# Kernel tuning notes

Hardware: AMD Instinct MI355X
Metric: run time of the kernel (lower is better)

The kernel has to match this reference:

```python
import jax, jax.numpy as jnp
import numpy as np

B, N, QD = 2, 4096, 512
HEADS, DIM_HEAD = 8, 64
INNER = HEADS * DIM_HEAD  # 512
SCALE = DIM_HEAD ** -0.5


def setup_inputs() -> dict:
    key = jax.random.key(0)
    ks = jax.random.split(key, 6)
    s = 0.02
    return {
        "x": jax.random.normal(ks[0], (B, N, QD), dtype=jnp.float32),
        "Wq": jax.random.normal(ks[1], (QD, INNER), dtype=jnp.float32) * s,
        "Wk": jax.random.normal(ks[2], (QD, INNER), dtype=jnp.float32) * s,
        "Wv": jax.random.normal(ks[3], (QD, INNER), dtype=jnp.float32) * s,
        "Wo": jax.random.normal(ks[4], (INNER, QD), dtype=jnp.float32) * s,
        "bo": jnp.zeros((QD,), dtype=jnp.float32),
    }


def reference(x, Wq, Wk, Wv, Wo, bo):
    # self-attention: context = x; mask = None; attention_sf = False
    q = x @ Wq  # [B, N, INNER]
    k = x @ Wk
    v = x @ Wv
    # split heads: [B, H, N, D]
    def split(t):
        return t.reshape(B, N, HEADS, DIM_HEAD).transpose(0, 2, 1, 3)
    q, k, v = split(q), split(k), split(v)
    # fp32 QK^T (ATTN_PRECISION='fp32' path)
    sim = jnp.einsum('bhid,bhjd->bhij', q.astype(jnp.float32), k.astype(jnp.float32)) * SCALE
    attn = jax.nn.softmax(sim, axis=-1)
    out = jnp.einsum('bhij,bhjd->bhid', attn, v)  # [B, H, N, D]
    out = out.transpose(0, 2, 1, 3).reshape(B, N, INNER)
    return out @ Wo + bo  # Dropout(p=0) is identity
```

## Files before the change

kernel.cpp:

```cpp
#include <hip/hip_runtime.h>
#include <hip/hip_bf16.h>


typedef __attribute__((ext_vector_type(8))) short short8;
typedef __attribute__((ext_vector_type(4))) float floatx4;
typedef __attribute__((ext_vector_type(16))) float floatx16;

#define MFMA16(a, b, c) __builtin_amdgcn_mfma_f32_16x16x32_bf16((a), (b), (c), 0, 0, 0)
#define MFMA32(a, b, c) __builtin_amdgcn_mfma_f32_32x32x16_bf16((a), (b), (c), 0, 0, 0)

#if __has_builtin(__builtin_amdgcn_exp2f)
#define EXP2(x) __builtin_amdgcn_exp2f(x)
#else
#define EXP2(x) exp2f(x)
#endif

#define QSCALE 0.18033688011112042f

static __device__ __forceinline__ unsigned short f2b(float f) {
  unsigned int u = __float_as_uint(f);
  u += 0x7FFFu + ((u >> 16) & 1u);
  return (unsigned short)(u >> 16);
}

static __device__ __forceinline__ unsigned int pkb(float a, float b) {
  float2 t{a, b};
  __hip_bfloat162 h = __float22bfloat162_rn(t);
  union { __hip_bfloat162 h2; unsigned int u; } cv;
  cv.h2 = h;
  return cv.u;
}

static __device__ __forceinline__ void dma16(const unsigned short* g,
                                             unsigned short* l) {
  __builtin_amdgcn_global_load_lds(
      (const __attribute__((address_space(1))) unsigned int*)g,
      (__attribute__((address_space(3))) unsigned int*)l, 16, 0, 0);
}

__global__ __launch_bounds__(256) void prep_kernel(
    const float* __restrict__ Wq, const float* __restrict__ Wk,
    const float* __restrict__ Wv, const float* __restrict__ Wo,
    const float* __restrict__ x, unsigned short* __restrict__ wtq,
    unsigned short* __restrict__ wtk, unsigned short* __restrict__ wtv,
    unsigned short* __restrict__ wto, unsigned short* __restrict__ xb) {
  const int z = blockIdx.z;
  const int tid = threadIdx.x;
  if (z >= 4) {
    const int bid = (z - 4) * 256 + blockIdx.y * 16 + blockIdx.x;
    const int idx = (bid * 256 + tid) * 8;
    const float4 a = *(const float4*)(x + idx);
    const float4 b = *(const float4*)(x + idx + 4);
    unsigned int u[4] = {pkb(a.x, a.y), pkb(a.z, a.w), pkb(b.x, b.y),
                         pkb(b.z, b.w)};
    *(short8*)(xb + idx) = *(short8*)u;
    return;
  }
  const float* __restrict__ W = (z == 0) ? Wq : (z == 1) ? Wk : (z == 2) ? Wv : Wo;
  unsigned short* __restrict__ T = (z == 0) ? wtq : (z == 1) ? wtk : (z == 2) ? wtv : wto;
  const int k0 = blockIdx.x * 32, c0 = blockIdx.y * 32;
  __shared__ float Ts[32][33];
  const int r = tid >> 3, cc = (tid & 7) * 4;
  const float4 v = *(const float4*)(W + (k0 + r) * 512 + c0 + cc);
  Ts[r][cc] = v.x; Ts[r][cc + 1] = v.y; Ts[r][cc + 2] = v.z; Ts[r][cc + 3] = v.w;
  __syncthreads();
  const unsigned long long uu =
      (unsigned long long)pkb(Ts[cc][r], Ts[cc + 1][r]) |
      ((unsigned long long)pkb(Ts[cc + 2][r], Ts[cc + 3][r]) << 32);
  *(unsigned long long*)(T + (c0 + r) * 512 + k0 + cc) = uu;
}

__global__ __launch_bounds__(256) void qkv_fused_kernel(
    const unsigned short* __restrict__ xb, const unsigned short* __restrict__ wtq,
    const unsigned short* __restrict__ wtk,
    const unsigned short* __restrict__ wtv, unsigned short* __restrict__ qo,
    unsigned short* __restrict__ ko, unsigned short* __restrict__ vo) {
  const int m0 = blockIdx.x * 128;
  const int c0 = blockIdx.y * 32;
  __shared__ __align__(16) unsigned short As[2][128 * 64];
  __shared__ __align__(16) unsigned short Bs[2][3][32 * 64];
  const int tid = threadIdx.x;
  const int lane = tid & 63, w = tid >> 6;
  const int i = lane & 15, q = lane >> 4;
  const int sl = i & 7;
  const int dr = lane >> 3, dc = lane & 7;
  const int sch = (dc ^ dr) * 8;
  const unsigned short* ag = xb + (m0 + w * 32 + dr) * 512 + sch;
  const unsigned short* bg[3];
  bg[0] = wtq + (c0 + w * 8 + dr) * 512 + sch;
  bg[1] = wtk + (c0 + w * 8 + dr) * 512 + sch;
  bg[2] = wtv + (c0 + w * 8 + dr) * 512 + sch;

  floatx4 acc[3][2][2] = {};

#pragma unroll
  for (int p = 0; p < 4; ++p) dma16(ag + p * 8 * 512, &As[0][(w * 32 + p * 8) * 64]);
#pragma unroll
  for (int z = 0; z < 3; ++z) dma16(bg[z], &Bs[0][z][(w * 8) * 64]);
  __syncthreads();

  int buf = 0;
  for (int ks = 0; ks < 8; ++ks) {
    if (ks < 7) {
      const int k1 = (ks + 1) * 64;
#pragma unroll
      for (int p = 0; p < 4; ++p)
        dma16(ag + p * 8 * 512 + k1, &As[buf ^ 1][(w * 32 + p * 8) * 64]);
#pragma unroll
      for (int z = 0; z < 3; ++z)
        dma16(bg[z] + k1, &Bs[buf ^ 1][z][(w * 8) * 64]);
    }
#pragma unroll
    for (int kc = 0; kc < 2; ++kc) {
      short8 af[2];
#pragma unroll
      for (int t = 0; t < 2; ++t)
        af[t] = *(const short8*)&As[buf][(w * 32 + t * 16 + i) * 64 +
                                        (((kc * 4 + q) ^ sl) * 8)];
#pragma unroll
      for (int z = 0; z < 3; ++z)
#pragma unroll
        for (int g = 0; g < 2; ++g) {
          const short8 bf = *(const short8*)&Bs[buf][z][(g * 16 + i) * 64 +
                                                        (((kc * 4 + q) ^ sl) * 8)];
#pragma unroll
          for (int t = 0; t < 2; ++t)
            acc[z][t][g] = MFMA16(af[t], bf, acc[z][t][g]);
        }
    }
    __syncthreads();
    buf ^= 1;
  }
#pragma unroll
  for (int z = 0; z < 3; ++z)
#pragma unroll
    for (int t = 0; t < 2; ++t)
#pragma unroll
      for (int g = 0; g < 2; ++g) {
        const int col = c0 + g * 16 + i;
        const int h = col >> 6, d = col & 63;
        const int row0 = m0 + w * 32 + t * 16 + q * 4;
        const int b = row0 >> 12;
        const int n0 = row0 & 4095;
        if (z == 2) {
          unsigned int* dst =
              (unsigned int*)&vo[(((b * 8 + h) * 64 + d) << 12) + n0];
          dst[0] = pkb(acc[z][t][g][0], acc[z][t][g][1]);
          dst[1] = pkb(acc[z][t][g][2], acc[z][t][g][3]);
        } else {
          unsigned short* dst = (z == 0) ? qo : ko;
          const float sc = (z == 0) ? QSCALE : 1.0f;
#pragma unroll
          for (int r = 0; r < 4; ++r)
            dst[(((b * 8 + h) << 12) + (n0 + r)) * 64 + d] =
                f2b(acc[z][t][g][r] * sc);
        }
      }
}

__global__ __launch_bounds__(512, 4) void flash_kernel(
    const unsigned short* __restrict__ Q, const unsigned short* __restrict__ K,
    const unsigned short* __restrict__ Vt, unsigned short* __restrict__ O) {
  const int bh = blockIdx.x;
  const int m0 = blockIdx.y * 128;
  const int tid = threadIdx.x;
  const int lane = tid & 63, w = tid >> 6;
  const int ql = lane & 31, hi = lane >> 5;
  const int rt = w & 3;
  const int kg = w >> 2;
  const unsigned short* qp = Q + bh * (4096 * 64);
  const unsigned short* kp = K + bh * (4096 * 64);
  const unsigned short* vp = Vt + bh * (64 * 4096);

  __shared__ __align__(16) unsigned short SM[32768];
  unsigned short* Ksb = SM + kg * 4096;
  unsigned short* Vsb = SM + 16384 + kg * 4096;

  const int srow = (tid & 255) >> 3;
  const int c0s = tid & 7;
  const int sw8 = (c0s ^ (srow & 7)) * 8;
  const unsigned short* kgp = kp + (kg * 2048 + srow) * 64 + c0s * 8;
  const unsigned short* vgp = vp + srow * 4096 + kg * 2048 + c0s * 8;

  short8 qf[4];
  {
    const unsigned short* qrp = qp + (m0 + rt * 32 + ql) * 64 + hi * 8;
#pragma unroll
    for (int ks = 0; ks < 4; ++ks) qf[ks] = *(const short8*)(qrp + ks * 16);
  }

  floatx16 accO[2] = {};
  float accLp = 0.f;
  const int sx = ql & 7;

  *(short8*)&Ksb[srow * 64 + sw8] = *(const short8*)(kgp);
  *(short8*)&Ksb[(srow + 32) * 64 + sw8] = *(const short8*)(kgp + 32 * 64);
  *(short8*)&Vsb[srow * 64 + sw8] = *(const short8*)(vgp);
  *(short8*)&Vsb[(srow + 32) * 64 + sw8] = *(const short8*)(vgp + 32 * 4096);
  __syncthreads();

  int buf = 0;
  for (int jt = 0; jt < 32; ++jt) {
    short8 kn0, kn1, vn0, vn1;
    if (jt < 31) {
      kn0 = *(const short8*)(kgp + (jt + 1) * 4096);
      kn1 = *(const short8*)(kgp + (jt + 1) * 4096 + 32 * 64);
      vn0 = *(const short8*)(vgp + (jt + 1) * 64);
      vn1 = *(const short8*)(vgp + (jt + 1) * 64 + 32 * 4096);
    }
    const unsigned short* Ks = Ksb + buf * 8192;
    const unsigned short* Vs = Vsb + buf * 8192;

    short8 pa[4];
#pragma unroll
    for (int kt = 0; kt < 2; ++kt) {
      floatx16 c;
#pragma unroll
      for (int j = 0; j < 16; ++j) c[j] = 0.0f;
      __builtin_amdgcn_s_setprio(1);
#pragma unroll
      for (int ks = 0; ks < 4; ++ks) {
        const short8 kf = *(const short8*)&Ks[(kt * 32 + ql) * 64 +
                                             (((2 * ks + hi) ^ sx) * 8)];
        c = MFMA32(kf, qf[ks], c);
      }
      __builtin_amdgcn_s_setprio(0);
      float e[16];
#pragma unroll
      for (int j = 0; j < 16; ++j) e[j] = EXP2(c[j]);
      accLp += (((e[0] + e[1]) + (e[2] + e[3])) +
                ((e[4] + e[5]) + (e[6] + e[7]))) +
               (((e[8] + e[9]) + (e[10] + e[11])) +
                ((e[12] + e[13]) + (e[14] + e[15])));
#pragma unroll
      for (int s2 = 0; s2 < 2; ++s2) {
        unsigned int a0 = pkb(e[8 * s2 + 0], e[8 * s2 + 1]);
        unsigned int c1 = pkb(e[8 * s2 + 2], e[8 * s2 + 3]);
        unsigned int b0 = pkb(e[8 * s2 + 4], e[8 * s2 + 5]);
        unsigned int d1 = pkb(e[8 * s2 + 6], e[8 * s2 + 7]);
        asm("v_permlane32_swap_b32 %0, %1" : "+v"(a0), "+v"(b0));
        asm("v_permlane32_swap_b32 %0, %1" : "+v"(c1), "+v"(d1));
        union { unsigned int u[4]; short8 s; } cv;
        cv.u[0] = a0; cv.u[1] = c1; cv.u[2] = b0; cv.u[3] = d1;
        pa[kt * 2 + s2] = cv.s;
      }
    }
    __builtin_amdgcn_s_setprio(1);
#pragma unroll
    for (int dt = 0; dt < 2; ++dt)
#pragma unroll
      for (int ks2 = 0; ks2 < 4; ++ks2) {
        const short8 vf = *(const short8*)&Vs[(dt * 32 + ql) * 64 +
                                              (((2 * ks2 + hi) ^ sx) * 8)];
        accO[dt] = MFMA32(pa[ks2], vf, accO[dt]);
      }
    __builtin_amdgcn_s_setprio(0);
    if (jt < 31) {
      unsigned short* Kw = Ksb + (buf ^ 1) * 8192;
      unsigned short* Vw = Vsb + (buf ^ 1) * 8192;
      *(short8*)&Kw[srow * 64 + sw8] = kn0;
      *(short8*)&Kw[(srow + 32) * 64 + sw8] = kn1;
      *(short8*)&Vw[srow * 64 + sw8] = vn0;
      *(short8*)&Vw[(srow + 32) * 64 + sw8] = vn1;
    }
    __syncthreads();
    buf ^= 1;
  }

  float* MB = (float*)SM;
  if (kg == 1) {
    float* dst = MB + (rt * 64 + lane) * 40;
#pragma unroll
    for (int dt = 0; dt < 2; ++dt)
#pragma unroll
      for (int r = 0; r < 16; ++r) dst[dt * 16 + r] = accO[dt][r];
    dst[32] = accLp;
  }
  __syncthreads();
  if (kg == 1) return;
  {
    const float* src = MB + (rt * 64 + lane) * 40;
#pragma unroll
    for (int dt = 0; dt < 2; ++dt)
#pragma unroll
      for (int r = 0; r < 16; ++r) accO[dt][r] += src[dt * 16 + r];
    accLp += src[32];
  }

  const float Lfull = accLp + __shfl(accLp, lane ^ 32, 64);
  const float invL = 1.0f / Lfull;
  const int b = bh >> 3, h = bh & 7;
#pragma unroll
  for (int r = 0; r < 16; ++r) {
    const int qrow = (r & 3) + 8 * (r >> 2) + 4 * hi;
    const float iv = __shfl(invL, qrow, 64);
    const int n = m0 + rt * 32 + qrow;
#pragma unroll
    for (int dt = 0; dt < 2; ++dt) {
      const int col = h * 64 + dt * 32 + ql;
      O[((b << 12) + n) * 512 + col] = f2b(accO[dt][r] * iv);
    }
  }
}

__global__ __launch_bounds__(256) void out_proj_kernel(
    const unsigned short* __restrict__ A, const unsigned short* __restrict__ wto,
    const float* __restrict__ bo, float* __restrict__ out) {
  const int m0 = blockIdx.x * 64, c0 = blockIdx.y * 64;
  __shared__ __align__(16) unsigned short As[2][64 * 64];
  __shared__ __align__(16) unsigned short Bs[2][64 * 64];
  const int tid = threadIdx.x;
  const int lane = tid & 63, w = tid >> 6;
  const int i = lane & 15, q = lane >> 4;
  const int wy = w >> 1, wx = w & 1;
  const int sl = i & 7;
  const int dr = lane >> 3, dc = lane & 7;
  const int sch = (dc ^ dr) * 8;
  const unsigned short* ag = A + (m0 + w * 16 + dr) * 512 + sch;
  const unsigned short* bg = wto + (c0 + w * 16 + dr) * 512 + sch;

  floatx4 acc[2][2] = {};
#pragma unroll
  for (int p = 0; p < 2; ++p) {
    dma16(ag + p * 8 * 512, &As[0][(w * 16 + p * 8) * 64]);
    dma16(bg + p * 8 * 512, &Bs[0][(w * 16 + p * 8) * 64]);
  }
  __syncthreads();

  int buf = 0;
  for (int ks = 0; ks < 8; ++ks) {
    if (ks < 7) {
      const int k1 = (ks + 1) * 64;
#pragma unroll
      for (int p = 0; p < 2; ++p) {
        dma16(ag + p * 8 * 512 + k1, &As[buf ^ 1][(w * 16 + p * 8) * 64]);
        dma16(bg + p * 8 * 512 + k1, &Bs[buf ^ 1][(w * 16 + p * 8) * 64]);
      }
    }
#pragma unroll
    for (int kc = 0; kc < 2; ++kc) {
      short8 af[2], bfr[2];
#pragma unroll
      for (int t = 0; t < 2; ++t)
        af[t] = *(const short8*)&As[buf][(wy * 32 + t * 16 + i) * 64 +
                                        (((kc * 4 + q) ^ sl) * 8)];
#pragma unroll
      for (int g = 0; g < 2; ++g)
        bfr[g] = *(const short8*)&Bs[buf][(wx * 32 + g * 16 + i) * 64 +
                                          (((kc * 4 + q) ^ sl) * 8)];
#pragma unroll
      for (int t = 0; t < 2; ++t)
#pragma unroll
        for (int g = 0; g < 2; ++g) acc[t][g] = MFMA16(af[t], bfr[g], acc[t][g]);
    }
    __syncthreads();
    buf ^= 1;
  }
#pragma unroll
  for (int t = 0; t < 2; ++t)
#pragma unroll
    for (int g = 0; g < 2; ++g) {
      const int col = c0 + wx * 32 + g * 16 + i;
      const float bias = bo[col];
#pragma unroll
      for (int r = 0; r < 4; ++r) {
        const int row = m0 + wy * 32 + t * 16 + q * 4 + r;
        out[row * 512 + col] = acc[t][g][r] + bias;
      }
    }
}

extern "C" void kernel_launch(void* const* d_in, const int* in_sizes, int n_in,
                              void* d_out, int out_size, void* d_ws,
                              size_t ws_size, hipStream_t stream) {
  const float* x = (const float*)d_in[0];
  const float* Wq = (const float*)d_in[1];
  const float* Wk = (const float*)d_in[2];
  const float* Wv = (const float*)d_in[3];
  const float* Wo = (const float*)d_in[4];
  const float* bo = (const float*)d_in[5];
  float* out = (float*)d_out;

  const size_t tsz = (size_t)16 * 4096 * 64;
  unsigned short* qws = (unsigned short*)d_ws;
  unsigned short* kws = qws + tsz;
  unsigned short* vws = kws + tsz;
  unsigned short* ows = vws + tsz;
  unsigned short* wtq = ows + tsz;
  unsigned short* wtk = wtq + 512 * 512;
  unsigned short* wtv = wtk + 512 * 512;
  unsigned short* wto = wtv + 512 * 512;
  unsigned short* xb = wto + 512 * 512;

  prep_kernel<<<dim3(16, 16, 12), 256, 0, stream>>>(Wq, Wk, Wv, Wo, x, wtq,
                                                    wtk, wtv, wto, xb);
  qkv_fused_kernel<<<dim3(64, 16), 256, 0, stream>>>(xb, wtq, wtk, wtv, qws,
                                                     kws, vws);
  flash_kernel<<<dim3(16, 32), 512, 0, stream>>>(qws, kws, vws, ows);
  out_proj_kernel<<<dim3(128, 8), 256, 0, stream>>>(ows, wto, bo, out);
}
```

Before: 194.2 us.

## Halve flash block to 4 waves with 64 query rows each and DMA tile loads

Rewrites the flash attention kernel to use 256 threads where each wave handles two 32-row query tiles, reusing each K fragment read from LDS across both tiles. K/V staging switches from register-staged global loads to direct global-to-LDS copies (dma16). The aim is to cut LDS read traffic and register staging cost per query row, in exchange for higher register pressure per wave and fewer waves per block for hiding latency.

```diff
diff --git a/kernel.cpp b/kernel.cpp
--- a/kernel.cpp
+++ b/kernel.cpp
@@ -158,7 +158,7 @@
       }
 }
 
-__global__ __launch_bounds__(512, 4) void flash_kernel(
+__global__ __launch_bounds__(256, 2) void flash_kernel(
     const unsigned short* __restrict__ Q, const unsigned short* __restrict__ K,
     const unsigned short* __restrict__ Vt, unsigned short* __restrict__ O) {
   const int bh = blockIdx.x;
@@ -166,139 +166,152 @@
   const int tid = threadIdx.x;
   const int lane = tid & 63, w = tid >> 6;
   const int ql = lane & 31, hi = lane >> 5;
-  const int rt = w & 3;
-  const int kg = w >> 2;
+  const int wq = w >> 1;
+  const int kg = w & 1;
   const unsigned short* qp = Q + bh * (4096 * 64);
   const unsigned short* kp = K + bh * (4096 * 64);
   const unsigned short* vp = Vt + bh * (64 * 4096);
 
   __shared__ __align__(16) unsigned short SM[32768];
-  unsigned short* Ksb = SM + kg * 4096;
-  unsigned short* Vsb = SM + 16384 + kg * 4096;
-
-  const int srow = (tid & 255) >> 3;
-  const int c0s = tid & 7;
-  const int sw8 = (c0s ^ (srow & 7)) * 8;
-  const unsigned short* kgp = kp + (kg * 2048 + srow) * 64 + c0s * 8;
-  const unsigned short* vgp = vp + srow * 4096 + kg * 2048 + c0s * 8;
-
-  short8 qf[4];
-  {
-    const unsigned short* qrp = qp + (m0 + rt * 32 + ql) * 64 + hi * 8;
-#pragma unroll
-    for (int ks = 0; ks < 4; ++ks) qf[ks] = *(const short8*)(qrp + ks * 16);
-  }
-
-  floatx16 accO[2] = {};
-  float accLp = 0.f;
+  unsigned short* Ks = SM;
+  unsigned short* Vs = SM + 16384;
+
+  const int rso = lane >> 3;
+  const int cso = ((lane & 7) ^ rso) * 8;
+  const unsigned short* ksrc = kp + (wq * 64 + kg * 32 + rso) * 64 + cso;
+  const unsigned short* vsrc = vp + (kg * 32 + rso) * 4096 + wq * 64 + cso;
+  unsigned short* kdst = Ks + wq * 4096 + kg * 2048;
+  unsigned short* vdst = Vs + wq * 4096 + kg * 2048;
+
+  short8 qf[2][4];
+#pragma unroll
+  for (int qt = 0; qt < 2; ++qt)
+#pragma unroll
+    for (int ks = 0; ks < 4; ++ks)
+      qf[qt][ks] = *(const short8*)(qp + (m0 + wq * 64 + qt * 32 + ql) * 64 +
+                                    ks * 16 + hi * 8);
+
+  floatx16 accO[2][2] = {};
+  float accLp[2] = {0.f, 0.f};
   const int sx = ql & 7;
 
-  *(short8*)&Ksb[srow * 64 + sw8] = *(const short8*)(kgp);
-  *(short8*)&Ksb[(srow + 32) * 64 + sw8] = *(const short8*)(kgp + 32 * 64);
-  *(short8*)&Vsb[srow * 64 + sw8] = *(const short8*)(vgp);
-  *(short8*)&Vsb[(srow + 32) * 64 + sw8] = *(const short8*)(vgp + 32 * 4096);
+#pragma unroll
+  for (int p = 0; p < 4; ++p) {
+    dma16(ksrc + p * 512, kdst + p * 512);
+    dma16(vsrc + p * 32768, vdst + p * 512);
+  }
   __syncthreads();
 
   int buf = 0;
   for (int jt = 0; jt < 32; ++jt) {
-    short8 kn0, kn1, vn0, vn1;
     if (jt < 31) {
-      kn0 = *(const short8*)(kgp + (jt + 1) * 4096);
-      kn1 = *(const short8*)(kgp + (jt + 1) * 4096 + 32 * 64);
-      vn0 = *(const short8*)(vgp + (jt + 1) * 64);
-      vn1 = *(const short8*)(vgp + (jt + 1) * 64 + 32 * 4096);
-    }
-    const unsigned short* Ks = Ksb + buf * 8192;
-    const unsigned short* Vs = Vsb + buf * 8192;
-
-    short8 pa[4];
+      const int jn = jt + 1;
+#pragma unroll
+      for (int p = 0; p < 4; ++p) {
+        dma16(ksrc + jn * 8192 + p * 512, kdst + (buf ^ 1) * 8192 + p * 512);
+        dma16(vsrc + jn * 128 + p * 32768, vdst + (buf ^ 1) * 8192 + p * 512);
+      }
+    }
+    const unsigned short* Kr = Ks + buf * 8192 + kg * 4096;
+    const unsigned short* Vr = Vs + buf * 8192 + kg * 4096;
+
+    short8 pa[2][4];
 #pragma unroll
     for (int kt = 0; kt < 2; ++kt) {
-      floatx16 c;
-#pragma unroll
-      for (int j = 0; j < 16; ++j) c[j] = 0.0f;
-      __builtin_amdgcn_s_setprio(1);
-#pragma unroll
-      for (int ks = 0; ks < 4; ++ks) {
-        const short8 kf = *(const short8*)&Ks[(kt * 32 + ql) * 64 +
-                                             (((2 * ks + hi) ^ sx) * 8)];
-        c = MFMA32(kf, qf[ks], c);
-      }
-      __builtin_amdgcn_s_setprio(0);
-      float e[16];
-#pragma unroll
-      for (int j = 0; j < 16; ++j) e[j] = EXP2(c[j]);
-      accLp += (((e[0] + e[1]) + (e[2] + e[3])) +
-                ((e[4] + e[5]) + (e[6] + e[7]))) +
-               (((e[8] + e[9]) + (e[10] + e[11])) +
-                ((e[12] + e[13]) + (e[14] + e[15])));
-#pragma unroll
-      for (int s2 = 0; s2 < 2; ++s2) {
-        unsigned int a0 = pkb(e[8 * s2 + 0], e[8 * s2 + 1]);
-        unsigned int c1 = pkb(e[8 * s2 + 2], e[8 * s2 + 3]);
-        unsigned int b0 = pkb(e[8 * s2 + 4], e[8 * s2 + 5]);
-        unsigned int d1 = pkb(e[8 * s2 + 6], e[8 * s2 + 7]);
-        asm("v_permlane32_swap_b32 %0, %1" : "+v"(a0), "+v"(b0));
-        asm("v_permlane32_swap_b32 %0, %1" : "+v"(c1), "+v"(d1));
-        union { unsigned int u[4]; short8 s; } cv;
-        cv.u[0] = a0; cv.u[1] = c1; cv.u[2] = b0; cv.u[3] = d1;
-        pa[kt * 2 + s2] = cv.s;
+      short8 kf[4];
+#pragma unroll
+      for (int ks = 0; ks < 4; ++ks)
+        kf[ks] = *(const short8*)&Kr[(kt * 32 + ql) * 64 +
+                                     (((2 * ks + hi) ^ sx) * 8)];
+#pragma unroll
+      for (int qt = 0; qt < 2; ++qt) {
+        floatx16 c;
+#pragma unroll
+        for (int j = 0; j < 16; ++j) c[j] = 0.0f;
+        __builtin_amdgcn_s_setprio(1);
+#pragma unroll
+        for (int ks = 0; ks < 4; ++ks) c = MFMA32(kf[ks], qf[qt][ks], c);
+        __builtin_amdgcn_s_setprio(0);
+        float e[16];
+#pragma unroll
+        for (int j = 0; j < 16; ++j) e[j] = EXP2(c[j]);
+        accLp[qt] += (((e[0] + e[1]) + (e[2] + e[3])) +
+                      ((e[4] + e[5]) + (e[6] + e[7]))) +
+                     (((e[8] + e[9]) + (e[10] + e[11])) +
+                      ((e[12] + e[13]) + (e[14] + e[15])));
+#pragma unroll
+        for (int s2 = 0; s2 < 2; ++s2) {
+          unsigned int a0 = pkb(e[8 * s2 + 0], e[8 * s2 + 1]);
+          unsigned int c1 = pkb(e[8 * s2 + 2], e[8 * s2 + 3]);
+          unsigned int b0 = pkb(e[8 * s2 + 4], e[8 * s2 + 5]);
+          unsigned int d1 = pkb(e[8 * s2 + 6], e[8 * s2 + 7]);
+          asm("v_permlane32_swap_b32 %0, %1" : "+v"(a0), "+v"(b0));
+          asm("v_permlane32_swap_b32 %0, %1" : "+v"(c1), "+v"(d1));
+          union { unsigned int u[4]; short8 s; } cv;
+          cv.u[0] = a0; cv.u[1] = c1; cv.u[2] = b0; cv.u[3] = d1;
+          pa[qt][kt * 2 + s2] = cv.s;
+        }
       }
     }
     __builtin_amdgcn_s_setprio(1);
 #pragma unroll
     for (int dt = 0; dt < 2; ++dt)
 #pragma unroll
-      for (int ks2 = 0; ks2 < 4; ++ks2) {
-        const short8 vf = *(const short8*)&Vs[(dt * 32 + ql) * 64 +
-                                              (((2 * ks2 + hi) ^ sx) * 8)];
-        accO[dt] = MFMA32(pa[ks2], vf, accO[dt]);
+      for (int kstep = 0; kstep < 4; ++kstep) {
+        const short8 vf = *(const short8*)&Vr[(dt * 32 + ql) * 64 +
+                                              (((2 * kstep + hi) ^ sx) * 8)];
+#pragma unroll
+        for (int qt = 0; qt < 2; ++qt)
+          accO[qt][dt] = MFMA32(pa[qt][kstep], vf, accO[qt][dt]);
       }
     __builtin_amdgcn_s_setprio(0);
-    if (jt < 31) {
-      unsigned short* Kw = Ksb + (buf ^ 1) * 8192;
-      unsigned short* Vw = Vsb + (buf ^ 1) * 8192;
-      *(short8*)&Kw[srow * 64 + sw8] = kn0;
-      *(short8*)&Kw[(srow + 32) * 64 + sw8] = kn1;
-      *(short8*)&Vw[srow * 64 + sw8] = vn0;
-      *(short8*)&Vw[(srow + 32) * 64 + sw8] = vn1;
-    }
     __syncthreads();
     buf ^= 1;
   }
 
   float* MB = (float*)SM;
   if (kg == 1) {
-    float* dst = MB + (rt * 64 + lane) * 40;
-#pragma unroll
-    for (int dt = 0; dt < 2; ++dt)
-#pragma unroll
-      for (int r = 0; r < 16; ++r) dst[dt * 16 + r] = accO[dt][r];
-    dst[32] = accLp;
+    float* dst = MB + (wq * 64 + lane) * 67;
+#pragma unroll
+    for (int qt = 0; qt < 2; ++qt)
+#pragma unroll
+      for (int dt = 0; dt < 2; ++dt)
+#pragma unroll
+        for (int r = 0; r < 16; ++r)
+          dst[qt * 32 + dt * 16 + r] = accO[qt][dt][r];
+    dst[64] = accLp[0];
+    dst[65] = accLp[1];
   }
   __syncthreads();
   if (kg == 1) return;
   {
-    const float* src = MB + (rt * 64 + lane) * 40;
-#pragma unroll
-    for (int dt = 0; dt < 2; ++dt)
-#pragma unroll
-      for (int r = 0; r < 16; ++r) accO[dt][r] += src[dt * 16 + r];
-    accLp += src[32];
-  }
-
-  const float Lfull = accLp + __shfl(accLp, lane ^ 32, 64);
-  const float invL = 1.0f / Lfull;
+    const float* src = MB + (wq * 64 + lane) * 67;
+#pragma unroll
+    for (int qt = 0; qt < 2; ++qt)
+#pragma unroll
+      for (int dt = 0; dt < 2; ++dt)
+#pragma unroll
+        for (int r = 0; r < 16; ++r)
+          accO[qt][dt][r] += src[qt * 32 + dt * 16 + r];
+    accLp[0] += src[64];
+    accLp[1] += src[65];
+  }
+
   const int b = bh >> 3, h = bh & 7;
 #pragma unroll
-  for (int r = 0; r < 16; ++r) {
-    const int qrow = (r & 3) + 8 * (r >> 2) + 4 * hi;
-    const float iv = __shfl(invL, qrow, 64);
-    const int n = m0 + rt * 32 + qrow;
-#pragma unroll
-    for (int dt = 0; dt < 2; ++dt) {
-      const int col = h * 64 + dt * 32 + ql;
-      O[((b << 12) + n) * 512 + col] = f2b(accO[dt][r] * iv);
+  for (int qt = 0; qt < 2; ++qt) {
+    const float Lfull = accLp[qt] + __shfl(accLp[qt], lane ^ 32, 64);
+    const float invL = 1.0f / Lfull;
+#pragma unroll
+    for (int r = 0; r < 16; ++r) {
+      const int qrow = (r & 3) + 8 * (r >> 2) + 4 * hi;
+      const float iv = __shfl(invL, qrow, 64);
+      const int n = m0 + wq * 64 + qt * 32 + qrow;
+#pragma unroll
+      for (int dt = 0; dt < 2; ++dt) {
+        const int col = h * 64 + dt * 32 + ql;
+        O[((b << 12) + n) * 512 + col] = f2b(accO[qt][dt][r] * iv);
+      }
     }
   }
 }
@@ -396,6 +409,6 @@
                                                     wtk, wtv, wto, xb);
   qkv_fused_kernel<<<dim3(64, 16), 256, 0, stream>>>(xb, wtq, wtk, wtv, qws,
                                                      kws, vws);
-  flash_kernel<<<dim3(16, 32), 512, 0, stream>>>(qws, kws, vws, ows);
+  flash_kernel<<<dim3(16, 32), 256, 0, stream>>>(qws, kws, vws, ows);
   out_proj_kernel<<<dim3(128, 8), 256, 0, stream>>>(ows, wto, bo, out);
 }
```

After: 195.1 us. About the same (+0.5%).
